# Kernel optimization log

Hardware: AMD Instinct MI355X
Metric: run time of the kernel (lower is better)

The kernel has to match this reference:

```python
import jax, jax.numpy as jnp
import numpy as np

N_NODES = 50000
N_EDGES = 600000
D = 128
DROP_P = 0.5


def setup_inputs() -> dict:
    key = jax.random.key(0)
    k1, k2, k3, k4, k5, k6 = jax.random.split(key, 6)
    x = jax.random.normal(k1, (N_NODES, D), dtype=jnp.float32)
    W = jax.random.normal(k2, (D, D), dtype=jnp.float32) * (1.0 / np.sqrt(D))
    b = jax.random.normal(k3, (D,), dtype=jnp.float32) * 0.01
    mask_u = jax.random.uniform(k4, (N_NODES, D), dtype=jnp.float32)
    src = jax.random.randint(k5, (N_EDGES,), 0, N_NODES, dtype=jnp.int64)
    dst = jax.random.randint(k6, (N_EDGES,), 0, N_NODES, dtype=jnp.int64)
    return {"x": x, "W": W, "b": b, "mask_u": mask_u, "src": src, "dst": dst}


def reference(x, W, b, mask_u, src, dst):
    n_nodes = x.shape[0]
    # linear + relu (nn.Linear stores weight as [out, in]; here W is [out, in])
    h = jax.nn.relu(jnp.einsum('nd,od->no', x, W) + b)
    # inverted dropout with precomputed uniform noise (train mode, p=0.5)
    keep = (mask_u >= DROP_P).astype(h.dtype)
    h = h * keep * (1.0 / (1.0 - DROP_P))
    # message passing: msg = h[src], reduce = sum over incoming edges per dst
    msgs = jnp.take(h, src, axis=0)            # [E, D] gather
    out = jax.ops.segment_sum(msgs, dst, num_segments=n_nodes)  # [N, D]
    return out
```

## Files before the change

kernel.cpp:

```cpp
#include <hip/hip_runtime.h>

#define D 128
#define TILE_N 16
#define HPITCH 132
#define RNODES 256
#define FCAP 48
#define LCAP 32
#define SPILL_MAX 8192

typedef __attribute__((ext_vector_type(8))) short  short8;
typedef __attribute__((ext_vector_type(4))) float  f32x4;

__device__ inline unsigned short f32_to_bf16(float f) {
    unsigned int u = __float_as_uint(f);
    unsigned int r = (u + 0x7FFFu + ((u >> 16) & 1u)) >> 16;
    return (unsigned short)r;
}
__device__ inline float bf16_to_f32(unsigned short s) {
    return __uint_as_float(((unsigned int)s) << 16);
}
__device__ inline short8 pack_bf16x8(float4 a, float4 b) {
    short8 u;
    u[0] = (short)f32_to_bf16(a.x); u[1] = (short)f32_to_bf16(a.y);
    u[2] = (short)f32_to_bf16(a.z); u[3] = (short)f32_to_bf16(a.w);
    u[4] = (short)f32_to_bf16(b.x); u[5] = (short)f32_to_bf16(b.y);
    u[6] = (short)f32_to_bf16(b.z); u[7] = (short)f32_to_bf16(b.w);
    return u;
}

__global__ __launch_bounds__(256) void zero_kernel(int* __restrict__ p, int n)
{
    int i = blockIdx.x * 256 + threadIdx.x;
    if (i < n) p[i] = 0;
}

__global__ __launch_bounds__(256) void prepbin_kernel(
    const float* __restrict__ W, unsigned short* __restrict__ Wb,
    const int* __restrict__ src, const int* __restrict__ dst,
    int n_edges, int chunk, int n_ranges,
    unsigned int* __restrict__ seg, int* __restrict__ cnt_grid,
    int* __restrict__ spill_cnt, int* __restrict__ spill)
{
    __shared__ __align__(16) char smem[50176];
    const int t = threadIdx.x;

    if ((int)blockIdx.x < n_ranges) {
        int* s_fcnt = (int*)smem;
        unsigned int* s_fifo = (unsigned int*)(smem + 1024);
        const int b  = blockIdx.x;
        const int nb = n_ranges;

        for (int i = t; i < n_ranges; i += 256) s_fcnt[i] = 0;
        __syncthreads();

        const int e0 = b * chunk;
        const int e1 = (e0 + chunk < n_edges) ? e0 + chunk : n_edges;
        for (int i = e0 + t; i < e1; i += 256) {
            int dd = dst[i];
            int ss = src[i];
            int r  = dd >> 8;
            int pos = atomicAdd(&s_fcnt[r], 1);
            if (pos < FCAP) {
                s_fifo[r * FCAP + pos] = ((unsigned)dd << 16) | (unsigned)ss;
            } else {
                int k = atomicAdd(spill_cnt, 1);
                if (k < SPILL_MAX) { spill[2 * k] = dd; spill[2 * k + 1] = ss; }
            }
        }
        __syncthreads();

        for (int f = t; f < n_ranges * FCAP; f += 256) {
            int r = f / FCAP, slot = f - r * FCAP;
            if (slot < s_fcnt[r])
                seg[((size_t)r * nb + b) * FCAP + slot] = s_fifo[f];
        }
        for (int r = t; r < n_ranges; r += 256) {
            int c = s_fcnt[r];
            cnt_grid[r * nb + b] = (c > FCAP) ? FCAP : c;
        }
    } else {
        const int bid = blockIdx.x - n_ranges;
        const int tid = bid * 256 + t;
        if (tid < (D * D) / 8) {
            float4 v0 = *(const float4*)&W[tid * 8];
            float4 v1 = *(const float4*)&W[tid * 8 + 4];
            *(short8*)&Wb[tid * 8] = pack_bf16x8(v0, v1);
        }
    }
}

__global__ __launch_bounds__(256, 8) void mega_kernel(
    const float* __restrict__ x, const unsigned short* __restrict__ Wb,
    const float* __restrict__ bias, const float* __restrict__ mask_u,
    unsigned short* __restrict__ h, int n_nodes,
    const unsigned int* __restrict__ seg, const int* __restrict__ cnt_grid,
    int nb1, int n_ranges,
    int* __restrict__ deg, unsigned short* __restrict__ bucket,
    int* __restrict__ spill_cnt, int* __restrict__ spill)
{
    __shared__ __align__(16) char smem[19712];
    const int t = threadIdx.x;

    if ((int)blockIdx.x < n_ranges) {
        int* s_pref = (int*)smem;
        int* s_cnt  = (int*)(smem + 1024);
        int* s_ncnt = (int*)(smem + 2048);
        unsigned short* s_slots = (unsigned short*)(smem + 3072);
        const int r = blockIdx.x;
        const unsigned rbase = (unsigned)r << 8;

        int v = (t < nb1) ? cnt_grid[r * nb1 + t] : 0;
        s_pref[t] = v;
        s_cnt[t]  = v;
        s_ncnt[t] = 0;
        __syncthreads();
        for (int o = 1; o < 256; o <<= 1) {
            int add = (t >= o) ? s_pref[t - o] : 0;
            __syncthreads();
            s_pref[t] += add;
            __syncthreads();
        }
        const int total = s_pref[255];

        for (int f = t; f < total; f += 256) {
            int lo = 0, hi = nb1 - 1;
            while (lo < hi) {
                int mid = (lo + hi) >> 1;
                if (s_pref[mid] > f) hi = mid; else lo = mid + 1;
            }
            int slot = f - (s_pref[lo] - s_cnt[lo]);
            unsigned pk = seg[((size_t)r * nb1 + lo) * FCAP + slot];
            unsigned dd = pk >> 16;
            unsigned ss = pk & 0xFFFFu;
            int rel = (int)(dd - rbase);
            int pos = atomicAdd(&s_ncnt[rel], 1);
            if (pos < LCAP) {
                s_slots[(rel << 5) + pos] = (unsigned short)ss;
            } else {
                int k = atomicAdd(spill_cnt, 1);
                if (k < SPILL_MAX) { spill[2 * k] = (int)dd; spill[2 * k + 1] = (int)ss; }
            }
        }
        __syncthreads();

        const int node = (int)rbase + t;
        if (node < n_nodes) {
            int c = s_ncnt[t];
            deg[node] = (c > LCAP) ? LCAP : c;
        }
        for (int vv = t; vv < 1024; vv += 256) {
            int rel = vv >> 2;
            int gn  = (int)rbase + rel;
            if (gn < n_nodes)
                *(short8*)&bucket[((size_t)gn << 5) + ((vv & 3) << 3)] =
                    *(const short8*)&s_slots[vv << 3];
        }
    } else {
        unsigned short* ht = (unsigned short*)smem;
        const int lane = t & 63;
        const int w    = t >> 6;
        const int fr   = lane & 15;
        const int fg   = lane >> 4;
        const int n0 = (blockIdx.x - n_ranges) * TILE_N;

        const int prow = t >> 4;
        const int pcg  = t & 15;
        const int pnode = n0 + prow;
        const bool pvalid = (pnode < n_nodes);
        const int mnode = pvalid ? pnode : (n_nodes - 1);
        const size_t moff = (size_t)mnode * D + pcg * 8;
        float4 m0 = *(const float4*)&mask_u[moff];
        float4 m1 = *(const float4*)&mask_u[moff + 4];

        int arow = n0 + fr;
        if (arow >= n_nodes) arow = n_nodes - 1;
        const float* xr = x + (size_t)arow * D;
        short8 a0 = pack_bf16x8(*(const float4*)&xr[ 0 + fg * 8],
                                *(const float4*)&xr[ 4 + fg * 8]);
        short8 a1 = pack_bf16x8(*(const float4*)&xr[32 + fg * 8],
                                *(const float4*)&xr[36 + fg * 8]);
        short8 a2 = pack_bf16x8(*(const float4*)&xr[64 + fg * 8],
                                *(const float4*)&xr[68 + fg * 8]);
        short8 a3 = pack_bf16x8(*(const float4*)&xr[96 + fg * 8],
                                *(const float4*)&xr[100 + fg * 8]);

        const float bs0 = bias[32 * w + fr];
        const float bs1 = bias[32 * w + 16 + fr];
        const unsigned short* wb0 = Wb + (size_t)(32 * w + fr) * D;
        const unsigned short* wb1 = Wb + (size_t)(32 * w + 16 + fr) * D;

        f32x4 acc0 = (f32x4){0.f, 0.f, 0.f, 0.f};
        f32x4 acc1 = (f32x4){0.f, 0.f, 0.f, 0.f};
        #pragma unroll
        for (int s = 0; s < 4; ++s) {
            short8 a = (s == 0) ? a0 : (s == 1) ? a1 : (s == 2) ? a2 : a3;
            short8 b0 = *(const short8*)&wb0[s * 32 + fg * 8];
            short8 b1 = *(const short8*)&wb1[s * 32 + fg * 8];
            acc0 = __builtin_amdgcn_mfma_f32_16x16x32_bf16(a, b0, acc0, 0, 0, 0);
            acc1 = __builtin_amdgcn_mfma_f32_16x16x32_bf16(a, b1, acc1, 0, 0, 0);
        }

        #pragma unroll
        for (int rr = 0; rr < 4; ++rr) {
            const int rl = fg * 4 + rr;
            float v0 = fmaxf(acc0[rr] + bs0, 0.f);
            float v1 = fmaxf(acc1[rr] + bs1, 0.f);
            ht[rl * HPITCH + 32 * w + fr]      = f32_to_bf16(v0);
            ht[rl * HPITCH + 32 * w + 16 + fr] = f32_to_bf16(v1);
        }
        __syncthreads();

        if (pvalid) {
            short8 hv = *(const short8*)&ht[prow * HPITCH + pcg * 8];
            short8 o;
            #pragma unroll
            for (int j = 0; j < 8; ++j) {
                float m = (j < 4) ? ((const float*)&m0)[j] : ((const float*)&m1)[j - 4];
                float v = bf16_to_f32((unsigned short)hv[j]) * 2.f;
                o[j] = (m >= 0.5f) ? (short)f32_to_bf16(v) : (short)0;
            }
            *(short8*)&h[(size_t)pnode * D + pcg * 8] = o;
        }
    }
}

__global__ __launch_bounds__(256) void gather_reduce_kernel(
    const unsigned short* __restrict__ h, const int* __restrict__ deg,
    const unsigned short* __restrict__ bucket, float* __restrict__ out,
    int n_nodes, const int* __restrict__ spill_cnt, const int* __restrict__ spill)
{
    const int t = threadIdx.x;
    const int node = blockIdx.x * 16 + (t >> 4);
    if (node >= n_nodes) return;
    const int cb = (t & 15) * 8;
    int dg = deg[node];
    if (dg > LCAP) dg = LCAP;
    const unsigned short* b = bucket + ((size_t)node << 5);

    float acc[8];
    #pragma unroll
    for (int j = 0; j < 8; ++j) acc[j] = 0.f;

    int i = 0;
    for (; i + 3 < dg; i += 4) {
        int s0 = b[i], s1 = b[i + 1], s2 = b[i + 2], s3 = b[i + 3];
        short8 v0 = *(const short8*)&h[(size_t)s0 * D + cb];
        short8 v1 = *(const short8*)&h[(size_t)s1 * D + cb];
        short8 v2 = *(const short8*)&h[(size_t)s2 * D + cb];
        short8 v3 = *(const short8*)&h[(size_t)s3 * D + cb];
        #pragma unroll
        for (int j = 0; j < 8; ++j)
            acc[j] += (bf16_to_f32((unsigned short)v0[j]) +
                       bf16_to_f32((unsigned short)v1[j])) +
                      (bf16_to_f32((unsigned short)v2[j]) +
                       bf16_to_f32((unsigned short)v3[j]));
    }
    for (; i < dg; ++i) {
        int s0 = b[i];
        short8 v0 = *(const short8*)&h[(size_t)s0 * D + cb];
        #pragma unroll
        for (int j = 0; j < 8; ++j) acc[j] += bf16_to_f32((unsigned short)v0[j]);
    }

    int nsp = *spill_cnt;
    if (nsp > 0) {
        if (nsp > SPILL_MAX) nsp = SPILL_MAX;
        for (int e = 0; e < nsp; ++e) {
            if (spill[2 * e] == node) {
                int ss = spill[2 * e + 1];
                short8 v = *(const short8*)&h[(size_t)ss * D + cb];
                #pragma unroll
                for (int j = 0; j < 8; ++j)
                    acc[j] += bf16_to_f32((unsigned short)v[j]);
            }
        }
    }

    f32x4 o0 = (f32x4){acc[0], acc[1], acc[2], acc[3]};
    f32x4 o1 = (f32x4){acc[4], acc[5], acc[6], acc[7]};
    __builtin_nontemporal_store(o0, (f32x4*)&out[(size_t)node * D + cb]);
    __builtin_nontemporal_store(o1, (f32x4*)&out[(size_t)node * D + cb + 4]);
}

__global__ __launch_bounds__(256) void gemm_fb_kernel(
    const float* __restrict__ x, const float* __restrict__ W,
    const float* __restrict__ bias, const float* __restrict__ mask_u,
    unsigned short* __restrict__ h, int n_nodes)
{
    int tid = blockIdx.x * 256 + threadIdx.x;
    if (tid >= n_nodes * 16) return;
    int node = tid >> 4, cg = tid & 15;
    for (int c = 0; c < 8; ++c) {
        int col = cg * 8 + c;
        float s = bias[col];
        for (int k = 0; k < D; ++k)
            s += bf16_to_f32(f32_to_bf16(x[(size_t)node * D + k])) *
                 bf16_to_f32(f32_to_bf16(W[(size_t)col * D + k]));
        s = fmaxf(s, 0.f);
        float m = mask_u[(size_t)node * D + col];
        s *= (m >= 0.5f) ? 2.f : 0.f;
        h[(size_t)node * D + col] = f32_to_bf16(s);
    }
}

__global__ __launch_bounds__(256) void scatter_atomic_kernel(
    const unsigned short* __restrict__ h, const int* __restrict__ src,
    const int* __restrict__ dst, float* __restrict__ out, int n_edges)
{
    const int t = threadIdx.x;
    const int e = blockIdx.x * 16 + (t >> 4);
    if (e >= n_edges) return;
    const int cb = (t & 15) * 8;
    const int s  = src[e];
    const int dd = dst[e];
    short8 v = *(const short8*)&h[(size_t)s * D + cb];
    float* o = &out[(size_t)dd * D + cb];
    #pragma unroll
    for (int j = 0; j < 8; ++j) atomicAdd(o + j, bf16_to_f32((unsigned short)v[j]));
}

extern "C" void kernel_launch(void* const* d_in, const int* in_sizes, int n_in,
                              void* d_out, int out_size, void* d_ws, size_t ws_size,
                              hipStream_t stream) {
    const float* x      = (const float*)d_in[0];
    const float* W      = (const float*)d_in[1];
    const float* bias   = (const float*)d_in[2];
    const float* mask_u = (const float*)d_in[3];
    const int*   src    = (const int*)d_in[4];
    const int*   dst    = (const int*)d_in[5];
    float* out = (float*)d_out;

    const int n_nodes  = in_sizes[0] / D;
    const int n_edges  = in_sizes[4];
    const int n_tiles  = (n_nodes + TILE_N - 1) / TILE_N;
    const int n_ranges = (n_nodes + RNODES - 1) / RNODES;
    const int nb1      = n_ranges;
    const int chunk    = (n_edges + nb1 - 1) / nb1;

    const size_t wb_bytes = (size_t)D * D * sizeof(unsigned short);
    const size_t h_bytes  = (size_t)n_nodes * D * sizeof(unsigned short);
    char* p = (char*)d_ws;
    unsigned short* Wb = (unsigned short*)p;     p += wb_bytes;
    unsigned short* h  = (unsigned short*)p;     p += h_bytes;
    int* deg       = (int*)p;                    p += (size_t)((n_nodes + 3) & ~3) * sizeof(int);
    int* spill_cnt = (int*)p;                    p += 16;
    int* spill     = (int*)p;                    p += (size_t)2 * SPILL_MAX * sizeof(int);
    unsigned short* bucket = (unsigned short*)p; p += (size_t)n_nodes * LCAP * sizeof(unsigned short);
    unsigned int* seg      = (unsigned int*)p;   p += (size_t)n_ranges * nb1 * FCAP * sizeof(unsigned int);
    int* cnt_grid  = (int*)p;                    p += (size_t)n_ranges * nb1 * sizeof(int);
    const size_t needed = (size_t)(p - (char*)d_ws);

    if (ws_size >= needed && n_nodes <= 65535) {
        zero_kernel<<<1, 256, 0, stream>>>(spill_cnt, 4);
        prepbin_kernel<<<n_ranges + 64, 256, 0, stream>>>(
            W, Wb, src, dst, n_edges, chunk, n_ranges,
            seg, cnt_grid, spill_cnt, spill);
        mega_kernel<<<n_ranges + n_tiles, 256, 0, stream>>>(
            x, Wb, bias, mask_u, h, n_nodes,
            seg, cnt_grid, nb1, n_ranges, deg, bucket, spill_cnt, spill);
        gather_reduce_kernel<<<(n_nodes + 15) / 16, 256, 0, stream>>>(
            h, deg, bucket, out, n_nodes, spill_cnt, spill);
    } else {
        unsigned short* hf = (unsigned short*)d_ws;
        gemm_fb_kernel<<<(n_nodes * 16 + 255) / 256, 256, 0, stream>>>(
            x, W, bias, mask_u, hf, n_nodes);
        zero_kernel<<<(out_size + 255) / 256, 256, 0, stream>>>((int*)d_out, out_size);
        scatter_atomic_kernel<<<(n_edges + 15) / 16, 256, 0, stream>>>(
            hf, src, dst, out, n_edges);
    }
}
```

Baseline: 76.04 us.

## Store h in permuted MFMA-native layout, drop LDS transpose, unroll gather by 8

The GEMM epilogue now applies bias, ReLU and dropout directly on MFMA accumulators and writes packed bf16 pairs in a permuted column order. This removes the LDS staging, the __syncthreads and the row-major transpose. The gather-reduce kernel un-permutes the columns when writing out, and its main loop is unrolled to 8 outstanding row loads for more memory-level parallelism. The trade-off is that the mask is now read with scalar loads and h is written with narrower 32-bit scattered stores.

```diff
diff --git a/kernel.cpp b/kernel.cpp
--- a/kernel.cpp
+++ b/kernel.cpp
@@ -2,7 +2,6 @@
 
 #define D 128
 #define TILE_N 16
-#define HPITCH 132
 #define RNODES 256
 #define FCAP 48
 #define LCAP 32
@@ -156,21 +155,21 @@
                     *(const short8*)&s_slots[vv << 3];
         }
     } else {
-        unsigned short* ht = (unsigned short*)smem;
         const int lane = t & 63;
-        const int w    = t >> 6;
+        const int q    = t >> 6;
         const int fr   = lane & 15;
         const int fg   = lane >> 4;
         const int n0 = (blockIdx.x - n_ranges) * TILE_N;
 
-        const int prow = t >> 4;
-        const int pcg  = t & 15;
-        const int pnode = n0 + prow;
-        const bool pvalid = (pnode < n_nodes);
-        const int mnode = pvalid ? pnode : (n_nodes - 1);
-        const size_t moff = (size_t)mnode * D + pcg * 8;
-        float4 m0 = *(const float4*)&mask_u[moff];
-        float4 m1 = *(const float4*)&mask_u[moff + 4];
+        float mk0[4], mk1[4];
+        #pragma unroll
+        for (int r = 0; r < 4; ++r) {
+            int nr = n0 + fg * 4 + r;
+            if (nr >= n_nodes) nr = n_nodes - 1;
+            const size_t mo = (size_t)nr * D + 32 * q + fr;
+            mk0[r] = mask_u[mo];
+            mk1[r] = mask_u[mo + 16];
+        }
 
         int arow = n0 + fr;
         if (arow >= n_nodes) arow = n_nodes - 1;
@@ -184,10 +183,10 @@
         short8 a3 = pack_bf16x8(*(const float4*)&xr[96 + fg * 8],
                                 *(const float4*)&xr[100 + fg * 8]);
 
-        const float bs0 = bias[32 * w + fr];
-        const float bs1 = bias[32 * w + 16 + fr];
-        const unsigned short* wb0 = Wb + (size_t)(32 * w + fr) * D;
-        const unsigned short* wb1 = Wb + (size_t)(32 * w + 16 + fr) * D;
+        const float bs0 = bias[32 * q + fr];
+        const float bs1 = bias[32 * q + 16 + fr];
+        const unsigned short* wb0 = Wb + (size_t)(32 * q + fr) * D;
+        const unsigned short* wb1 = Wb + (size_t)(32 * q + 16 + fr) * D;
 
         f32x4 acc0 = (f32x4){0.f, 0.f, 0.f, 0.f};
         f32x4 acc1 = (f32x4){0.f, 0.f, 0.f, 0.f};
@@ -200,26 +199,17 @@
             acc1 = __builtin_amdgcn_mfma_f32_16x16x32_bf16(a, b1, acc1, 0, 0, 0);
         }
 
-        #pragma unroll
-        for (int rr = 0; rr < 4; ++rr) {
-            const int rl = fg * 4 + rr;
-            float v0 = fmaxf(acc0[rr] + bs0, 0.f);
-            float v1 = fmaxf(acc1[rr] + bs1, 0.f);
-            ht[rl * HPITCH + 32 * w + fr]      = f32_to_bf16(v0);
-            ht[rl * HPITCH + 32 * w + 16 + fr] = f32_to_bf16(v1);
-        }
-        __syncthreads();
-
-        if (pvalid) {
-            short8 hv = *(const short8*)&ht[prow * HPITCH + pcg * 8];
-            short8 o;
-            #pragma unroll
-            for (int j = 0; j < 8; ++j) {
-                float m = (j < 4) ? ((const float*)&m0)[j] : ((const float*)&m1)[j - 4];
-                float v = bf16_to_f32((unsigned short)hv[j]) * 2.f;
-                o[j] = (m >= 0.5f) ? (short)f32_to_bf16(v) : (short)0;
-            }
-            *(short8*)&h[(size_t)pnode * D + pcg * 8] = o;
+        unsigned int* h32 = (unsigned int*)h;
+        #pragma unroll
+        for (int r = 0; r < 4; ++r) {
+            const int nr = n0 + fg * 4 + r;
+            if (nr < n_nodes) {
+                float v0 = fmaxf(acc0[r] + bs0, 0.f) * (mk0[r] >= 0.5f ? 2.f : 0.f);
+                float v1 = fmaxf(acc1[r] + bs1, 0.f) * (mk1[r] >= 0.5f ? 2.f : 0.f);
+                unsigned u = (unsigned)f32_to_bf16(v0) |
+                             ((unsigned)f32_to_bf16(v1) << 16);
+                h32[(size_t)nr * 64 + q * 16 + fr] = u;
+            }
         }
     }
 }
@@ -232,7 +222,8 @@
     const int t = threadIdx.x;
     const int node = blockIdx.x * 16 + (t >> 4);
     if (node >= n_nodes) return;
-    const int cb = (t & 15) * 8;
+    const int l16 = t & 15;
+    const int cb = l16 * 8;
     int dg = deg[node];
     if (dg > LCAP) dg = LCAP;
     const unsigned short* b = bucket + ((size_t)node << 5);
@@ -242,12 +233,31 @@
     for (int j = 0; j < 8; ++j) acc[j] = 0.f;
 
     int i = 0;
+    for (; i + 7 < dg; i += 8) {
+        short8 v0 = *(const short8*)&h[(size_t)b[i]     * D + cb];
+        short8 v1 = *(const short8*)&h[(size_t)b[i + 1] * D + cb];
+        short8 v2 = *(const short8*)&h[(size_t)b[i + 2] * D + cb];
+        short8 v3 = *(const short8*)&h[(size_t)b[i + 3] * D + cb];
+        short8 v4 = *(const short8*)&h[(size_t)b[i + 4] * D + cb];
+        short8 v5 = *(const short8*)&h[(size_t)b[i + 5] * D + cb];
+        short8 v6 = *(const short8*)&h[(size_t)b[i + 6] * D + cb];
+        short8 v7 = *(const short8*)&h[(size_t)b[i + 7] * D + cb];
+        #pragma unroll
+        for (int j = 0; j < 8; ++j)
+            acc[j] += ((bf16_to_f32((unsigned short)v0[j]) +
+                        bf16_to_f32((unsigned short)v1[j])) +
+                       (bf16_to_f32((unsigned short)v2[j]) +
+                        bf16_to_f32((unsigned short)v3[j]))) +
+                      ((bf16_to_f32((unsigned short)v4[j]) +
+                        bf16_to_f32((unsigned short)v5[j])) +
+                       (bf16_to_f32((unsigned short)v6[j]) +
+                        bf16_to_f32((unsigned short)v7[j])));
+    }
     for (; i + 3 < dg; i += 4) {
-        int s0 = b[i], s1 = b[i + 1], s2 = b[i + 2], s3 = b[i + 3];
-        short8 v0 = *(const short8*)&h[(size_t)s0 * D + cb];
-        short8 v1 = *(const short8*)&h[(size_t)s1 * D + cb];
-        short8 v2 = *(const short8*)&h[(size_t)s2 * D + cb];
-        short8 v3 = *(const short8*)&h[(size_t)s3 * D + cb];
+        short8 v0 = *(const short8*)&h[(size_t)b[i]     * D + cb];
+        short8 v1 = *(const short8*)&h[(size_t)b[i + 1] * D + cb];
+        short8 v2 = *(const short8*)&h[(size_t)b[i + 2] * D + cb];
+        short8 v3 = *(const short8*)&h[(size_t)b[i + 3] * D + cb];
         #pragma unroll
         for (int j = 0; j < 8; ++j)
             acc[j] += (bf16_to_f32((unsigned short)v0[j]) +
@@ -256,8 +266,7 @@
                        bf16_to_f32((unsigned short)v3[j]));
     }
     for (; i < dg; ++i) {
-        int s0 = b[i];
-        short8 v0 = *(const short8*)&h[(size_t)s0 * D + cb];
+        short8 v0 = *(const short8*)&h[(size_t)b[i] * D + cb];
         #pragma unroll
         for (int j = 0; j < 8; ++j) acc[j] += bf16_to_f32((unsigned short)v0[j]);
     }
@@ -276,10 +285,12 @@
         }
     }
 
-    f32x4 o0 = (f32x4){acc[0], acc[1], acc[2], acc[3]};
-    f32x4 o1 = (f32x4){acc[4], acc[5], acc[6], acc[7]};
-    __builtin_nontemporal_store(o0, (f32x4*)&out[(size_t)node * D + cb]);
-    __builtin_nontemporal_store(o1, (f32x4*)&out[(size_t)node * D + cb + 4]);
+    const int q  = l16 >> 2;
+    const int f0 = 4 * (l16 & 3);
+    f32x4 s1 = (f32x4){acc[0], acc[2], acc[4], acc[6]};
+    f32x4 s2 = (f32x4){acc[1], acc[3], acc[5], acc[7]};
+    __builtin_nontemporal_store(s1, (f32x4*)&out[(size_t)node * D + 32 * q + f0]);
+    __builtin_nontemporal_store(s2, (f32x4*)&out[(size_t)node * D + 32 * q + 16 + f0]);
 }
 
 __global__ __launch_bounds__(256) void gemm_fb_kernel(
```

Result: faster. 73.67 us (-3.1%).
